# Kernel optimization log

Measured on AMD Instinct MI355X. Metric: run time of the kernel, lower is better.

Reference implementation:

```python
import jax, jax.numpy as jnp
import numpy as np

N, L, C_IN, DEM = 64, 2048, 256, 10


def setup_inputs() -> dict:
    key = jax.random.key(0)
    k1, k2, k3, k4 = jax.random.split(key, 4)
    timesteps = jax.random.normal(k1, (N, L, C_IN), dtype=jnp.float32)
    dem = jax.random.normal(k2, (N, DEM), dtype=jnp.float32)
    W1 = jax.random.normal(k3, (DEM, 40), dtype=jnp.float32) * 0.1
    b1 = jnp.zeros((40,), dtype=jnp.float32)
    W2 = jax.random.normal(k4, (40, 20), dtype=jnp.float32) * 0.1
    b2 = jnp.zeros((20,), dtype=jnp.float32)
    return {"timesteps": timesteps, "dem": dem, "W1": W1, "b1": b1, "W2": W2, "b2": b2}


def reference(timesteps, dem, W1, b1, W2, b2):
    # dem MLP: Linear(10,40) -> ReLU -> (Dropout p=0, eval) -> Linear(40,20) -> ReLU
    h = jax.nn.relu(dem @ W1 + b1)
    dem_emb = jax.nn.relu(h @ W2 + b2)                     # (N, 20)
    n, l, _ = timesteps.shape
    dem_b = jnp.broadcast_to(dem_emb[:, None, :], (n, l, dem_emb.shape[-1]))
    x = jnp.concatenate([timesteps, dem_b], axis=-1)       # (N, L, C)
    # Causal nonzero-average pool: avg_pool1d with kernel=L over (L-1)-left-padded
    # sequence == at step t, sum(x[:t+1]) / count_nonzero(x[:t+1]) per channel.
    csum = jnp.cumsum(x, axis=1)                           # (N, L, C)
    ccnt = jnp.cumsum((x != 0).astype(x.dtype), axis=1)    # (N, L, C)
    p_avg = csum / jnp.maximum(ccnt, 1.0)
    return jax.nn.relu(p_avg)
```

## Files before the change

### kernel.cpp

```cpp
#include <hip/hip_runtime.h>


#define NB 64
#define LL 2048
#define CIN 256
#define COUT 276
#define DEMD 10
#define H1 40
#define H2 20
#define SEG 64
#define LSEG (LL / SEG)
#define UB 8
#define NBATCH (LSEG / UB)

typedef float vfloat4 __attribute__((ext_vector_type(4)));

static __device__ __forceinline__ void nt_store4(float* p, float4 v) {
    vfloat4 t = {v.x, v.y, v.z, v.w};
    __builtin_nontemporal_store(t, (vfloat4*)p);
}

__global__ __launch_bounds__(256) void pme_partials(
    const float* __restrict__ ts,
    float* __restrict__ part)
{
    const int tid  = threadIdx.x;
    const int w    = tid >> 6;
    const int lane = tid & 63;

    const int unit = blockIdx.x * 4 + w;
    const int seg  = unit & (SEG - 1);
    const int n    = unit >> 6;

    const float4* tp = (const float4*)(ts + ((size_t)n * LL + seg * LSEG) * CIN) + lane;

    float4 sum = make_float4(0.f, 0.f, 0.f, 0.f);
    float4 cnt = make_float4(0.f, 0.f, 0.f, 0.f);

    float4 v[2][UB];
#pragma unroll
    for (int u = 0; u < UB; ++u)
        v[0][u] = tp[(size_t)u * (CIN / 4)];

    for (int bb = 0; bb < NBATCH; ++bb) {
        const int cur = bb & 1;
        if (bb + 1 < NBATCH) {
#pragma unroll
            for (int u = 0; u < UB; ++u)
                v[cur ^ 1][u] = tp[(size_t)((bb + 1) * UB + u) * (CIN / 4)];
        }
#pragma unroll
        for (int u = 0; u < UB; ++u) {
            float4 x = v[cur][u];
            sum.x += x.x; cnt.x += (x.x != 0.f) ? 1.f : 0.f;
            sum.y += x.y; cnt.y += (x.y != 0.f) ? 1.f : 0.f;
            sum.z += x.z; cnt.z += (x.z != 0.f) ? 1.f : 0.f;
            sum.w += x.w; cnt.w += (x.w != 0.f) ? 1.f : 0.f;
        }
    }

    float4* pp = (float4*)part + ((size_t)n * SEG + seg) * 128 + lane * 2;
    pp[0] = make_float4(sum.x, cnt.x, sum.y, cnt.y);
    pp[1] = make_float4(sum.z, cnt.z, sum.w, cnt.w);
}

__global__ __launch_bounds__(256) void pme_prefix(
    float* __restrict__ part)
{
    const int tid  = threadIdx.x;
    const int w    = tid >> 6;
    const int lane = tid & 63;
    const int n    = blockIdx.x * 4 + w;

    float4* p = (float4*)part + (size_t)n * SEG * 128 + lane * 2;

    float4 ra = make_float4(0.f, 0.f, 0.f, 0.f);
    float4 rb = make_float4(0.f, 0.f, 0.f, 0.f);
    for (int s = 0; s < SEG; ++s) {
        float4 a = p[(size_t)s * 128];
        float4 b = p[(size_t)s * 128 + 1];
        p[(size_t)s * 128]     = ra;
        p[(size_t)s * 128 + 1] = rb;
        ra.x += a.x; ra.y += a.y; ra.z += a.z; ra.w += a.w;
        rb.x += b.x; rb.y += b.y; rb.z += b.z; rb.w += b.w;
    }
}

__global__ __launch_bounds__(256) void pme_scan(
    const float* __restrict__ ts,
    const float* __restrict__ part,
    const float* __restrict__ dem,
    const float* __restrict__ W1, const float* __restrict__ b1,
    const float* __restrict__ W2, const float* __restrict__ b2,
    float* __restrict__ out)
{
    const int tid  = threadIdx.x;
    const int w    = tid >> 6;
    const int lane = tid & 63;

    const int unit = blockIdx.x * 4 + w;
    const int seg  = unit & (SEG - 1);
    const int n    = unit >> 6;

    const float* dn = dem + n * DEMD;
    float h[H1];
#pragma unroll
    for (int k = 0; k < H1; ++k) {
        float hk = b1[k];
#pragma unroll
        for (int i = 0; i < DEMD; ++i)
            hk += dn[i] * W1[i * H1 + k];
        h[k] = fmaxf(hk, 0.f);
    }
    float4 e4q = make_float4(0.f, 0.f, 0.f, 0.f);
    {
        const int q = (lane < 5) ? lane : 0;
        float e0 = b2[q * 4 + 0], e1 = b2[q * 4 + 1], e2 = b2[q * 4 + 2], e3 = b2[q * 4 + 3];
#pragma unroll
        for (int k = 0; k < H1; ++k) {
            e0 += h[k] * W2[k * H2 + q * 4 + 0];
            e1 += h[k] * W2[k * H2 + q * 4 + 1];
            e2 += h[k] * W2[k * H2 + q * 4 + 2];
            e3 += h[k] * W2[k * H2 + q * 4 + 3];
        }
        e4q = make_float4(fmaxf(e0, 0.f), fmaxf(e1, 0.f), fmaxf(e2, 0.f), fmaxf(e3, 0.f));
    }

    const float4* pp = (const float4*)part + ((size_t)n * SEG + seg) * 128 + lane * 2;
    float4 a  = pp[0];
    float4 bq = pp[1];
    float4 acc = make_float4(a.x,  a.z,  bq.x, bq.z);
    float4 cnt = make_float4(a.y,  a.w,  bq.y, bq.w);

    const float4* tp = (const float4*)(ts + ((size_t)n * LL + seg * LSEG) * CIN) + lane;
    float* oprow = out + ((size_t)n * LL + seg * LSEG) * COUT;

    float4 v[2][UB];
#pragma unroll
    for (int u = 0; u < UB; ++u)
        v[0][u] = tp[(size_t)u * (CIN / 4)];

    for (int bb = 0; bb < NBATCH; ++bb) {
        const int cur = bb & 1;
        if (bb + 1 < NBATCH) {
#pragma unroll
            for (int u = 0; u < UB; ++u)
                v[cur ^ 1][u] = tp[(size_t)((bb + 1) * UB + u) * (CIN / 4)];
        }
#pragma unroll
        for (int u = 0; u < UB; ++u) {
            float4 x = v[cur][u];
            float4 r;
            acc.x += x.x; cnt.x += (x.x != 0.f) ? 1.f : 0.f;
            acc.y += x.y; cnt.y += (x.y != 0.f) ? 1.f : 0.f;
            acc.z += x.z; cnt.z += (x.z != 0.f) ? 1.f : 0.f;
            acc.w += x.w; cnt.w += (x.w != 0.f) ? 1.f : 0.f;
            r.x = fmaxf(acc.x * __builtin_amdgcn_rcpf(fmaxf(cnt.x, 1.f)), 0.f);
            r.y = fmaxf(acc.y * __builtin_amdgcn_rcpf(fmaxf(cnt.y, 1.f)), 0.f);
            r.z = fmaxf(acc.z * __builtin_amdgcn_rcpf(fmaxf(cnt.z, 1.f)), 0.f);
            r.w = fmaxf(acc.w * __builtin_amdgcn_rcpf(fmaxf(cnt.w, 1.f)), 0.f);
            float* rowp = oprow + (size_t)(bb * UB + u) * COUT;
            nt_store4(rowp + lane * 4, r);
            if (lane < 5)
                nt_store4(rowp + CIN + lane * 4, e4q);
        }
    }
}

extern "C" void kernel_launch(void* const* d_in, const int* in_sizes, int n_in,
                              void* d_out, int out_size, void* d_ws, size_t ws_size,
                              hipStream_t stream) {
    const float* ts  = (const float*)d_in[0];
    const float* dem = (const float*)d_in[1];
    const float* W1  = (const float*)d_in[2];
    const float* b1  = (const float*)d_in[3];
    const float* W2  = (const float*)d_in[4];
    const float* b2  = (const float*)d_in[5];
    float* out  = (float*)d_out;
    float* part = (float*)d_ws;

    pme_partials<<<(NB * SEG) / 4, 256, 0, stream>>>(ts, part);
    pme_prefix<<<NB / 4, 256, 0, stream>>>(part);
    pme_scan<<<(NB * SEG) / 4, 256, 0, stream>>>(ts, part, dem, W1, b1, W2, b2, out);
}
```

Baseline: 299.0 us.

## Fuse three-pass scan into single kernel with chained decoupled lookback

Replaces the partials/prefix/scan kernel sequence with one fused kernel. Blocks take tiles in dynamic order from an atomic ticket, and each segment waits on its predecessor's flag to get the inclusive prefix before running the output pass. Segment count drops from 64 to 32 per sequence, and the timesteps tile is re-read right after the partial sum, so the second read is more likely to hit cache. This removes two kernel launches and the serial prefix kernel, at the cost of a serial chain of spin-waits across segments and a memset before each launch.

```diff
diff --git a/kernel.cpp b/kernel.cpp
--- a/kernel.cpp
+++ b/kernel.cpp
@@ -8,10 +8,13 @@
 #define DEMD 10
 #define H1 40
 #define H2 20
-#define SEG 64
-#define LSEG (LL / SEG)
-#define UB 8
-#define NBATCH (LSEG / UB)
+
+#define FSEG 32
+#define FLSEG (LL / FSEG)
+#define FUB 8
+#define FNB (FLSEG / FUB)
+#define NUNITS (NB * FSEG)
+#define NBLK (NUNITS / 4)
 
 typedef float vfloat4 __attribute__((ext_vector_type(4)));
 
@@ -20,100 +23,106 @@
     __builtin_nontemporal_store(t, (vfloat4*)p);
 }
 
-__global__ __launch_bounds__(256) void pme_partials(
+static __device__ __forceinline__ unsigned long long packsc(float s, float c) {
+    union { float f[2]; unsigned long long u; } t;
+    t.f[0] = s; t.f[1] = c;
+    return t.u;
+}
+
+static __device__ __forceinline__ float2 unpacksc(unsigned long long u) {
+    union { float f[2]; unsigned long long uu; } t;
+    t.uu = u;
+    return make_float2(t.f[0], t.f[1]);
+}
+
+__global__ __launch_bounds__(256) void pme_fused(
     const float* __restrict__ ts,
-    float* __restrict__ part)
+    const float* __restrict__ dem,
+    const float* __restrict__ W1, const float* __restrict__ b1,
+    const float* __restrict__ W2, const float* __restrict__ b2,
+    float* __restrict__ out,
+    unsigned int* __restrict__ tick,
+    unsigned int* __restrict__ flags,
+    unsigned long long* __restrict__ payload)
 {
+    __shared__ unsigned int s_t;
+    if (threadIdx.x == 0)
+        s_t = atomicAdd(tick, 1u) & (NBLK - 1);
+    __syncthreads();
+
     const int tid  = threadIdx.x;
     const int w    = tid >> 6;
     const int lane = tid & 63;
+    const int g    = (int)s_t * 4 + w;
+    const int n    = g & (NB - 1);
+    const int seg  = g >> 6;
 
-    const int unit = blockIdx.x * 4 + w;
-    const int seg  = unit & (SEG - 1);
-    const int n    = unit >> 6;
-
-    const float4* tp = (const float4*)(ts + ((size_t)n * LL + seg * LSEG) * CIN) + lane;
+    const float4* tp = (const float4*)(ts + ((size_t)n * LL + seg * FLSEG) * CIN) + lane;
 
     float4 sum = make_float4(0.f, 0.f, 0.f, 0.f);
-    float4 cnt = make_float4(0.f, 0.f, 0.f, 0.f);
-
-    float4 v[2][UB];
+    float4 ctv = make_float4(0.f, 0.f, 0.f, 0.f);
+    {
+        float4 v[2][FUB];
 #pragma unroll
-    for (int u = 0; u < UB; ++u)
-        v[0][u] = tp[(size_t)u * (CIN / 4)];
-
-    for (int bb = 0; bb < NBATCH; ++bb) {
-        const int cur = bb & 1;
-        if (bb + 1 < NBATCH) {
+        for (int u = 0; u < FUB; ++u)
+            v[0][u] = tp[(size_t)u * (CIN / 4)];
+        for (int bb = 0; bb < FNB; ++bb) {
+            const int cur = bb & 1;
+            if (bb + 1 < FNB) {
 #pragma unroll
-            for (int u = 0; u < UB; ++u)
-                v[cur ^ 1][u] = tp[(size_t)((bb + 1) * UB + u) * (CIN / 4)];
-        }
+                for (int u = 0; u < FUB; ++u)
+                    v[cur ^ 1][u] = tp[(size_t)((bb + 1) * FUB + u) * (CIN / 4)];
+            }
 #pragma unroll
-        for (int u = 0; u < UB; ++u) {
-            float4 x = v[cur][u];
-            sum.x += x.x; cnt.x += (x.x != 0.f) ? 1.f : 0.f;
-            sum.y += x.y; cnt.y += (x.y != 0.f) ? 1.f : 0.f;
-            sum.z += x.z; cnt.z += (x.z != 0.f) ? 1.f : 0.f;
-            sum.w += x.w; cnt.w += (x.w != 0.f) ? 1.f : 0.f;
+            for (int u = 0; u < FUB; ++u) {
+                float4 x = v[cur][u];
+                sum.x += x.x; ctv.x += (x.x != 0.f) ? 1.f : 0.f;
+                sum.y += x.y; ctv.y += (x.y != 0.f) ? 1.f : 0.f;
+                sum.z += x.z; ctv.z += (x.z != 0.f) ? 1.f : 0.f;
+                sum.w += x.w; ctv.w += (x.w != 0.f) ? 1.f : 0.f;
+            }
         }
     }
 
-    float4* pp = (float4*)part + ((size_t)n * SEG + seg) * 128 + lane * 2;
-    pp[0] = make_float4(sum.x, cnt.x, sum.y, cnt.y);
-    pp[1] = make_float4(sum.z, cnt.z, sum.w, cnt.w);
-}
-
-__global__ __launch_bounds__(256) void pme_prefix(
-    float* __restrict__ part)
-{
-    const int tid  = threadIdx.x;
-    const int w    = tid >> 6;
-    const int lane = tid & 63;
-    const int n    = blockIdx.x * 4 + w;
-
-    float4* p = (float4*)part + (size_t)n * SEG * 128 + lane * 2;
-
-    float4 ra = make_float4(0.f, 0.f, 0.f, 0.f);
-    float4 rb = make_float4(0.f, 0.f, 0.f, 0.f);
-    for (int s = 0; s < SEG; ++s) {
-        float4 a = p[(size_t)s * 128];
-        float4 b = p[(size_t)s * 128 + 1];
-        p[(size_t)s * 128]     = ra;
-        p[(size_t)s * 128 + 1] = rb;
-        ra.x += a.x; ra.y += a.y; ra.z += a.z; ra.w += a.w;
-        rb.x += b.x; rb.y += b.y; rb.z += b.z; rb.w += b.w;
+    float psum[4] = {0.f, 0.f, 0.f, 0.f};
+    float pcnt[4] = {0.f, 0.f, 0.f, 0.f};
+    if (seg > 0) {
+        const unsigned int* fl = flags + (n * FSEG + seg - 1);
+        while (__hip_atomic_load(fl, __ATOMIC_ACQUIRE, __HIP_MEMORY_SCOPE_AGENT) == 0u)
+            __builtin_amdgcn_s_sleep(2);
+        const unsigned long long* pp = payload + (size_t)(n * FSEG + seg - 1) * 256 + lane * 4;
+#pragma unroll
+        for (int j = 0; j < 4; ++j) {
+            float2 sc = unpacksc(__hip_atomic_load(pp + j, __ATOMIC_RELAXED, __HIP_MEMORY_SCOPE_AGENT));
+            psum[j] = sc.x; pcnt[j] = sc.y;
+        }
     }
-}
-
-__global__ __launch_bounds__(256) void pme_scan(
-    const float* __restrict__ ts,
-    const float* __restrict__ part,
-    const float* __restrict__ dem,
-    const float* __restrict__ W1, const float* __restrict__ b1,
-    const float* __restrict__ W2, const float* __restrict__ b2,
-    float* __restrict__ out)
-{
-    const int tid  = threadIdx.x;
-    const int w    = tid >> 6;
-    const int lane = tid & 63;
-
-    const int unit = blockIdx.x * 4 + w;
-    const int seg  = unit & (SEG - 1);
-    const int n    = unit >> 6;
+    if (seg < FSEG - 1) {
+        unsigned long long* ps = payload + (size_t)(n * FSEG + seg) * 256 + lane * 4;
+        const float ls[4] = {sum.x, sum.y, sum.z, sum.w};
+        const float lc[4] = {ctv.x, ctv.y, ctv.z, ctv.w};
+#pragma unroll
+        for (int j = 0; j < 4; ++j)
+            __hip_atomic_store(ps + j, packsc(psum[j] + ls[j], pcnt[j] + lc[j]),
+                               __ATOMIC_RELAXED, __HIP_MEMORY_SCOPE_AGENT);
+        __threadfence();
+        if (lane == 0)
+            __hip_atomic_store(flags + (n * FSEG + seg), 1u,
+                               __ATOMIC_RELEASE, __HIP_MEMORY_SCOPE_AGENT);
+    }
 
     const float* dn = dem + n * DEMD;
-    float h[H1];
-#pragma unroll
-    for (int k = 0; k < H1; ++k) {
-        float hk = b1[k];
-#pragma unroll
-        for (int i = 0; i < DEMD; ++i)
-            hk += dn[i] * W1[i * H1 + k];
-        h[k] = fmaxf(hk, 0.f);
-    }
     float4 e4q = make_float4(0.f, 0.f, 0.f, 0.f);
     {
+        float h[H1];
+#pragma unroll
+        for (int k = 0; k < H1; ++k) {
+            float hk = b1[k];
+#pragma unroll
+            for (int i = 0; i < DEMD; ++i)
+                hk += dn[i] * W1[i * H1 + k];
+            h[k] = fmaxf(hk, 0.f);
+        }
         const int q = (lane < 5) ? lane : 0;
         float e0 = b2[q * 4 + 0], e1 = b2[q * 4 + 1], e2 = b2[q * 4 + 2], e3 = b2[q * 4 + 3];
 #pragma unroll
@@ -126,29 +135,25 @@
         e4q = make_float4(fmaxf(e0, 0.f), fmaxf(e1, 0.f), fmaxf(e2, 0.f), fmaxf(e3, 0.f));
     }
 
-    const float4* pp = (const float4*)part + ((size_t)n * SEG + seg) * 128 + lane * 2;
-    float4 a  = pp[0];
-    float4 bq = pp[1];
-    float4 acc = make_float4(a.x,  a.z,  bq.x, bq.z);
-    float4 cnt = make_float4(a.y,  a.w,  bq.y, bq.w);
+    float4 acc = make_float4(psum[0], psum[1], psum[2], psum[3]);
+    float4 cnt = make_float4(pcnt[0], pcnt[1], pcnt[2], pcnt[3]);
 
-    const float4* tp = (const float4*)(ts + ((size_t)n * LL + seg * LSEG) * CIN) + lane;
-    float* oprow = out + ((size_t)n * LL + seg * LSEG) * COUT;
+    float* oprow = out + ((size_t)n * LL + seg * FLSEG) * COUT;
 
-    float4 v[2][UB];
+    float4 v[2][FUB];
 #pragma unroll
-    for (int u = 0; u < UB; ++u)
+    for (int u = 0; u < FUB; ++u)
         v[0][u] = tp[(size_t)u * (CIN / 4)];
 
-    for (int bb = 0; bb < NBATCH; ++bb) {
+    for (int bb = 0; bb < FNB; ++bb) {
         const int cur = bb & 1;
-        if (bb + 1 < NBATCH) {
+        if (bb + 1 < FNB) {
 #pragma unroll
-            for (int u = 0; u < UB; ++u)
-                v[cur ^ 1][u] = tp[(size_t)((bb + 1) * UB + u) * (CIN / 4)];
+            for (int u = 0; u < FUB; ++u)
+                v[cur ^ 1][u] = tp[(size_t)((bb + 1) * FUB + u) * (CIN / 4)];
         }
 #pragma unroll
-        for (int u = 0; u < UB; ++u) {
+        for (int u = 0; u < FUB; ++u) {
             float4 x = v[cur][u];
             float4 r;
             acc.x += x.x; cnt.x += (x.x != 0.f) ? 1.f : 0.f;
@@ -159,7 +164,7 @@
             r.y = fmaxf(acc.y * __builtin_amdgcn_rcpf(fmaxf(cnt.y, 1.f)), 0.f);
             r.z = fmaxf(acc.z * __builtin_amdgcn_rcpf(fmaxf(cnt.z, 1.f)), 0.f);
             r.w = fmaxf(acc.w * __builtin_amdgcn_rcpf(fmaxf(cnt.w, 1.f)), 0.f);
-            float* rowp = oprow + (size_t)(bb * UB + u) * COUT;
+            float* rowp = oprow + (size_t)(bb * FUB + u) * COUT;
             nt_store4(rowp + lane * 4, r);
             if (lane < 5)
                 nt_store4(rowp + CIN + lane * 4, e4q);
@@ -176,10 +181,14 @@
     const float* b1  = (const float*)d_in[3];
     const float* W2  = (const float*)d_in[4];
     const float* b2  = (const float*)d_in[5];
-    float* out  = (float*)d_out;
-    float* part = (float*)d_ws;
+    float* out = (float*)d_out;
+    float* ws  = (float*)d_ws;
 
-    pme_partials<<<(NB * SEG) / 4, 256, 0, stream>>>(ts, part);
-    pme_prefix<<<NB / 4, 256, 0, stream>>>(part);
-    pme_scan<<<(NB * SEG) / 4, 256, 0, stream>>>(ts, part, dem, W1, b1, W2, b2, out);
+    hipMemsetAsync(d_ws, 0, 16384, stream);
+
+    pme_fused<<<NBLK, 256, 0, stream>>>(
+        ts, dem, W1, b1, W2, b2, out,
+        (unsigned int*)ws,
+        (unsigned int*)(ws + 1024),
+        (unsigned long long*)(ws + 4096));
 }
```

Result: slower. 990.0 us (+231.0%).

## Fuse three-kernel segmented scan into one block-per-batch kernel with LDS prefix

Applied to the files above, without the earlier changes.

Replaces the partials, prefix and scan kernels with a single kernel where one 1024-thread block handles a whole batch row. Each of its 16 waves reduces 128 rows, exchanges partial sums and counts through shared memory, then rescans its rows and writes the output. This removes two kernel launches and the global-memory round trip for partials. In exchange the grid shrinks to 64 blocks, far fewer than the number of CUs on the GPU, so most of the device sits idle and memory bandwidth may be underused. Each wave also makes two serial passes over 128 rows. The small MLP now computes the hidden layer inline.

```diff
diff --git a/kernel.cpp b/kernel.cpp
--- a/kernel.cpp
+++ b/kernel.cpp
@@ -8,10 +8,11 @@
 #define DEMD 10
 #define H1 40
 #define H2 20
-#define SEG 64
-#define LSEG (LL / SEG)
+
+#define WAVES 16
+#define ROWS (LL / WAVES)
 #define UB 8
-#define NBATCH (LSEG / UB)
+#define NBATCH (ROWS / UB)
 
 typedef float vfloat4 __attribute__((ext_vector_type(4)));
 
@@ -20,120 +21,86 @@
     __builtin_nontemporal_store(t, (vfloat4*)p);
 }
 
-__global__ __launch_bounds__(256) void pme_partials(
+__global__ __launch_bounds__(1024) void pme_onepass(
     const float* __restrict__ ts,
-    float* __restrict__ part)
-{
-    const int tid  = threadIdx.x;
-    const int w    = tid >> 6;
-    const int lane = tid & 63;
-
-    const int unit = blockIdx.x * 4 + w;
-    const int seg  = unit & (SEG - 1);
-    const int n    = unit >> 6;
-
-    const float4* tp = (const float4*)(ts + ((size_t)n * LL + seg * LSEG) * CIN) + lane;
-
-    float4 sum = make_float4(0.f, 0.f, 0.f, 0.f);
-    float4 cnt = make_float4(0.f, 0.f, 0.f, 0.f);
-
-    float4 v[2][UB];
-#pragma unroll
-    for (int u = 0; u < UB; ++u)
-        v[0][u] = tp[(size_t)u * (CIN / 4)];
-
-    for (int bb = 0; bb < NBATCH; ++bb) {
-        const int cur = bb & 1;
-        if (bb + 1 < NBATCH) {
-#pragma unroll
-            for (int u = 0; u < UB; ++u)
-                v[cur ^ 1][u] = tp[(size_t)((bb + 1) * UB + u) * (CIN / 4)];
-        }
-#pragma unroll
-        for (int u = 0; u < UB; ++u) {
-            float4 x = v[cur][u];
-            sum.x += x.x; cnt.x += (x.x != 0.f) ? 1.f : 0.f;
-            sum.y += x.y; cnt.y += (x.y != 0.f) ? 1.f : 0.f;
-            sum.z += x.z; cnt.z += (x.z != 0.f) ? 1.f : 0.f;
-            sum.w += x.w; cnt.w += (x.w != 0.f) ? 1.f : 0.f;
-        }
-    }
-
-    float4* pp = (float4*)part + ((size_t)n * SEG + seg) * 128 + lane * 2;
-    pp[0] = make_float4(sum.x, cnt.x, sum.y, cnt.y);
-    pp[1] = make_float4(sum.z, cnt.z, sum.w, cnt.w);
-}
-
-__global__ __launch_bounds__(256) void pme_prefix(
-    float* __restrict__ part)
-{
-    const int tid  = threadIdx.x;
-    const int w    = tid >> 6;
-    const int lane = tid & 63;
-    const int n    = blockIdx.x * 4 + w;
-
-    float4* p = (float4*)part + (size_t)n * SEG * 128 + lane * 2;
-
-    float4 ra = make_float4(0.f, 0.f, 0.f, 0.f);
-    float4 rb = make_float4(0.f, 0.f, 0.f, 0.f);
-    for (int s = 0; s < SEG; ++s) {
-        float4 a = p[(size_t)s * 128];
-        float4 b = p[(size_t)s * 128 + 1];
-        p[(size_t)s * 128]     = ra;
-        p[(size_t)s * 128 + 1] = rb;
-        ra.x += a.x; ra.y += a.y; ra.z += a.z; ra.w += a.w;
-        rb.x += b.x; rb.y += b.y; rb.z += b.z; rb.w += b.w;
-    }
-}
-
-__global__ __launch_bounds__(256) void pme_scan(
-    const float* __restrict__ ts,
-    const float* __restrict__ part,
     const float* __restrict__ dem,
     const float* __restrict__ W1, const float* __restrict__ b1,
     const float* __restrict__ W2, const float* __restrict__ b2,
     float* __restrict__ out)
 {
+    __shared__ float4 LS[WAVES][64];
+    __shared__ float4 LC[WAVES][64];
+
     const int tid  = threadIdx.x;
     const int w    = tid >> 6;
     const int lane = tid & 63;
+    const int n    = blockIdx.x;
 
-    const int unit = blockIdx.x * 4 + w;
-    const int seg  = unit & (SEG - 1);
-    const int n    = unit >> 6;
+    const float4* tp = (const float4*)(ts + ((size_t)n * LL + w * ROWS) * CIN) + lane;
 
-    const float* dn = dem + n * DEMD;
-    float h[H1];
+    float4 sum = make_float4(0.f, 0.f, 0.f, 0.f);
+    float4 ctv = make_float4(0.f, 0.f, 0.f, 0.f);
+    {
+        float4 v[2][UB];
 #pragma unroll
-    for (int k = 0; k < H1; ++k) {
-        float hk = b1[k];
+        for (int u = 0; u < UB; ++u)
+            v[0][u] = tp[(size_t)u * (CIN / 4)];
+        for (int bb = 0; bb < NBATCH; ++bb) {
+            const int cur = bb & 1;
+            if (bb + 1 < NBATCH) {
+#pragma unroll
+                for (int u = 0; u < UB; ++u)
+                    v[cur ^ 1][u] = tp[(size_t)((bb + 1) * UB + u) * (CIN / 4)];
+            }
+#pragma unroll
+            for (int u = 0; u < UB; ++u) {
+                float4 x = v[cur][u];
+                sum.x += x.x; ctv.x += (x.x != 0.f) ? 1.f : 0.f;
+                sum.y += x.y; ctv.y += (x.y != 0.f) ? 1.f : 0.f;
+                sum.z += x.z; ctv.z += (x.z != 0.f) ? 1.f : 0.f;
+                sum.w += x.w; ctv.w += (x.w != 0.f) ? 1.f : 0.f;
+            }
+        }
+    }
+
+    LS[w][lane] = sum;
+    LC[w][lane] = ctv;
+    __syncthreads();
+
+    float4 acc = make_float4(0.f, 0.f, 0.f, 0.f);
+    float4 cnt = make_float4(0.f, 0.f, 0.f, 0.f);
+    for (int s = 0; s < w; ++s) {
+        float4 a = LS[s][lane];
+        float4 c = LC[s][lane];
+        acc.x += a.x; acc.y += a.y; acc.z += a.z; acc.w += a.w;
+        cnt.x += c.x; cnt.y += c.y; cnt.z += c.z; cnt.w += c.w;
+    }
+
+    float4 e4q;
+    {
+        const float* dn = dem + n * DEMD;
+        float d[DEMD];
 #pragma unroll
         for (int i = 0; i < DEMD; ++i)
-            hk += dn[i] * W1[i * H1 + k];
-        h[k] = fmaxf(hk, 0.f);
-    }
-    float4 e4q = make_float4(0.f, 0.f, 0.f, 0.f);
-    {
+            d[i] = dn[i];
         const int q = (lane < 5) ? lane : 0;
         float e0 = b2[q * 4 + 0], e1 = b2[q * 4 + 1], e2 = b2[q * 4 + 2], e3 = b2[q * 4 + 3];
 #pragma unroll
         for (int k = 0; k < H1; ++k) {
-            e0 += h[k] * W2[k * H2 + q * 4 + 0];
-            e1 += h[k] * W2[k * H2 + q * 4 + 1];
-            e2 += h[k] * W2[k * H2 + q * 4 + 2];
-            e3 += h[k] * W2[k * H2 + q * 4 + 3];
+            float hk = b1[k];
+#pragma unroll
+            for (int i = 0; i < DEMD; ++i)
+                hk += d[i] * W1[i * H1 + k];
+            hk = fmaxf(hk, 0.f);
+            e0 += hk * W2[k * H2 + q * 4 + 0];
+            e1 += hk * W2[k * H2 + q * 4 + 1];
+            e2 += hk * W2[k * H2 + q * 4 + 2];
+            e3 += hk * W2[k * H2 + q * 4 + 3];
         }
         e4q = make_float4(fmaxf(e0, 0.f), fmaxf(e1, 0.f), fmaxf(e2, 0.f), fmaxf(e3, 0.f));
     }
 
-    const float4* pp = (const float4*)part + ((size_t)n * SEG + seg) * 128 + lane * 2;
-    float4 a  = pp[0];
-    float4 bq = pp[1];
-    float4 acc = make_float4(a.x,  a.z,  bq.x, bq.z);
-    float4 cnt = make_float4(a.y,  a.w,  bq.y, bq.w);
-
-    const float4* tp = (const float4*)(ts + ((size_t)n * LL + seg * LSEG) * CIN) + lane;
-    float* oprow = out + ((size_t)n * LL + seg * LSEG) * COUT;
+    float* oprow = out + ((size_t)n * LL + w * ROWS) * COUT;
 
     float4 v[2][UB];
 #pragma unroll
@@ -176,10 +143,7 @@
     const float* b1  = (const float*)d_in[3];
     const float* W2  = (const float*)d_in[4];
     const float* b2  = (const float*)d_in[5];
-    float* out  = (float*)d_out;
-    float* part = (float*)d_ws;
+    float* out = (float*)d_out;
 
-    pme_partials<<<(NB * SEG) / 4, 256, 0, stream>>>(ts, part);
-    pme_prefix<<<NB / 4, 256, 0, stream>>>(part);
-    pme_scan<<<(NB * SEG) / 4, 256, 0, stream>>>(ts, part, dem, W1, b1, W2, b2, out);
+    pme_onepass<<<NB, 1024, 0, stream>>>(ts, dem, W1, b1, W2, b2, out);
 }
```

After: 426.5 us. +42.6%, slower.
